# Performance work log

Measured on AMD Instinct MI355X. Metric: run time of the kernel, lower is better.

Reference implementation:

```python
import jax, jax.numpy as jnp
import numpy as np

N = 4096      # nodes
IN = 45       # input_dim
H = 44        # hidden_dim
NH = 4        # num_heads
HD = H // NH  # head_dim = 11
E = 131072    # edges
SCALE = 0.1
NEG = -1e9


def _linear_params(key, fan_in, fan_out):
    kw, kb = jax.random.split(key)
    s = 1.0 / np.sqrt(fan_in)
    W = jax.random.uniform(kw, (fan_in, fan_out), jnp.float32, -s, s)
    b = jax.random.uniform(kb, (fan_out,), jnp.float32, -s, s)
    return W, b


def setup_inputs() -> dict:
    key = jax.random.key(0)
    ks = jax.random.split(key, 9)
    node_features = jax.random.normal(ks[0], (N, IN), jnp.float32)
    edge_index = jax.random.randint(ks[1], (2, E), 0, N, jnp.int32)
    # dt_minutes must be nonnegative (sqrt); channel 1 unused by forward
    temporal_data = jax.random.uniform(ks[2], (N, N, 2), jnp.float32, 0.01, 60.0)
    Wp, bp = _linear_params(ks[3], IN, H)
    Wq, bq = _linear_params(ks[4], H, H)
    Wk, bk = _linear_params(ks[5], H, H)
    Wv, bv = _linear_params(ks[6], H, H)
    Wo, bo = _linear_params(ks[7], H, H)
    return dict(node_features=node_features, edge_index=edge_index,
                temporal_data=temporal_data, Wp=Wp, bp=bp, Wq=Wq, bq=bq,
                Wk=Wk, bk=bk, Wv=Wv, bv=bv, Wo=Wo, bo=bo)


def reference(node_features, edge_index, temporal_data,
              Wp, bp, Wq, bq, Wk, bk, Wv, bv, Wo, bo):
    # input projection (N > 1000 so dag_positional_encoding is skipped)
    x = node_features @ Wp + bp                       # [N, H]
    # per-head QKV: [NH, N, HD]
    Q = (x @ Wq + bq).reshape(N, NH, HD).transpose(1, 0, 2)
    K = (x @ Wk + bk).reshape(N, NH, HD).transpose(1, 0, 2)
    V = (x @ Wv + bv).reshape(N, NH, HD).transpose(1, 0, 2)
    # edge mask: True blocks attention; edges and self-loops are allowed
    mask = jnp.ones((N, N), dtype=bool)
    mask = mask.at[edge_index[0], edge_index[1]].set(False)
    diag = jnp.arange(N)
    mask = mask.at[diag, diag].set(False)
    # rbf temporal bias: -sqrt(dt / (scale + 1e-6))
    tb = -jnp.sqrt(temporal_data[:, :, 0] / (SCALE + 1e-6))  # [N, N]
    scores = jnp.einsum('hnd,hmd->hnm', Q, K) / np.sqrt(HD)  # [NH, N, N]
    scores = scores + tb[None]
    scores = jnp.where(mask[None], NEG, scores)
    attn = jax.nn.softmax(scores, axis=-1)
    out = jnp.einsum('hnm,hmd->hnd', attn, V)                # [NH, N, HD]
    attended = out.transpose(1, 0, 2).reshape(N, H)          # [N, H]
    return attended @ Wo + bo
```

## Files before the change

kernel.cpp:

```cpp
#include <hip/hip_runtime.h>
#include <math.h>

#define NN 4096
#define INDIM 45
#define HH 44
#define NHEAD 4
#define HD 11
#define NEDGE 131072
#define CAP 128
#define MASKW (NN / 64)
#define NPB 8
#define RPITCH 66

typedef unsigned short ushort_t;

__device__ __forceinline__ float wsum64(float v) {
    #pragma unroll
    for (int i = 32; i > 0; i >>= 1) v += __shfl_xor(v, i, 64);
    return v;
}
__device__ __forceinline__ float wmax64(float v) {
    #pragma unroll
    for (int i = 32; i > 0; i >>= 1) v = fmaxf(v, __shfl_xor(v, i, 64));
    return v;
}
__device__ __forceinline__ ushort_t f2bf(float x) {
    unsigned u = __float_as_uint(x);
    u += 0x7FFFu + ((u >> 16) & 1u);
    return (ushort_t)(u >> 16);
}
__device__ __forceinline__ float bfl(unsigned u) { return __uint_as_float(u << 16); }
__device__ __forceinline__ float bfh(unsigned u) { return __uint_as_float(u & 0xFFFF0000u); }

__global__ __launch_bounds__(256)
void proj_zero(const float* __restrict__ nf,
               const float* __restrict__ Wp, const float* __restrict__ bp,
               const float* __restrict__ Wq, const float* __restrict__ bq,
               const float* __restrict__ Wk, const float* __restrict__ bk,
               const float* __restrict__ Wv, const float* __restrict__ bv,
               unsigned long long* __restrict__ mask,
               float* __restrict__ Qp, ushort_t* __restrict__ KVb) {
    const int tid = threadIdx.x;
    const int gsz = gridDim.x * 256;
    for (int i = blockIdx.x * 256 + tid; i < NN * MASKW; i += gsz) mask[i] = 0ull;

    __shared__ float xs[NPB][HH];
    const int n0 = blockIdx.x * NPB;
    for (int idx = tid; idx < NPB * HH; idx += 256) {
        int nl = idx / HH, j = idx - nl * HH;
        const float* row = nf + (size_t)(n0 + nl) * INDIM;
        float a = bp[j];
        #pragma unroll
        for (int k = 0; k < INDIM; ++k) a += row[k] * Wp[k * HH + j];
        xs[nl][j] = a;
    }
    __syncthreads();
    for (int idx = tid; idx < NPB * HH; idx += 256) {
        int nl = idx / HH, j = idx - nl * HH;
        const float* row = xs[nl];
        float aq = bq[j], ak = bk[j], av = bv[j];
        #pragma unroll
        for (int k = 0; k < HH; ++k) {
            float xv = row[k];
            aq += xv * Wq[k * HH + j];
            ak += xv * Wk[k * HH + j];
            av += xv * Wv[k * HH + j];
        }
        int h = j / HD, d = j - h * HD;
        size_t nh = (size_t)(n0 + nl) * NHEAD + h;
        Qp[nh * 12 + d]       = aq;
        KVb[nh * 24 + d]      = f2bf(ak);
        KVb[nh * 24 + 12 + d] = f2bf(av);
    }
}

__global__ __launch_bounds__(256)
void build_mask(const int* __restrict__ ei, unsigned long long* __restrict__ mask) {
    int i = blockIdx.x * blockDim.x + threadIdx.x;
    if (i < NEDGE) {
        int r = ei[i];
        int c = ei[NEDGE + i];
        atomicOr(&mask[(size_t)r * MASKW + (c >> 6)], 1ull << (c & 63));
    }
}

__global__ __launch_bounds__(256, 4)
void attn_out(const float* __restrict__ Qp, const ushort_t* __restrict__ KVb,
              const float* __restrict__ temporal,
              const unsigned long long* __restrict__ mask,
              const float* __restrict__ Wo, const float* __restrict__ bo,
              float* __restrict__ out) {
    const int tid = threadIdx.x;
    const int lane = tid & 63;
    const int h = tid >> 6;
    const int n = blockIdx.x;
    const float scale = 0.30151134457776363f;
    const float tbmul = 9.99990000099999f;

    __shared__ int cols_s[NHEAD][CAP];
    __shared__ float red_s[NHEAD][12][RPITCH];
    __shared__ float att_s[HH];

    unsigned long long w = mask[(size_t)n * MASKW + lane];
    if (lane == (n >> 6)) w |= 1ull << (n & 63);
    int c = __popcll(w);
    int inc = c;
    #pragma unroll
    for (int i = 1; i < 64; i <<= 1) {
        int v = __shfl_up(inc, i, 64);
        if (lane >= i) inc += v;
    }
    int off = inc - c;
    int deg = __shfl(inc, 63, 64);
    if (deg > CAP) deg = CAP;
    while (w) {
        int b = __builtin_ctzll(w);
        w &= w - 1;
        if (off < CAP) cols_s[h][off] = lane * 64 + b;
        ++off;
    }

    const float4* qp4 = (const float4*)(Qp + ((size_t)n * NHEAD + h) * 12);
    float4 q0 = qp4[0], q1 = qp4[1], q2 = qp4[2];

    if (deg <= 64) {
        const bool act = lane < deg;
        const int col = act ? cols_s[h][lane] : cols_s[h][0];
        float t = temporal[((size_t)n * NN + col) * 2];
        const uint4* kv4 = (const uint4*)(KVb + (size_t)(col * NHEAD + h) * 24);
        uint4 A = kv4[0], B = kv4[1], C = kv4[2];
        float s = q0.x*bfl(A.x) + q0.y*bfh(A.x) + q0.z*bfl(A.y) + q0.w*bfh(A.y)
                + q1.x*bfl(A.z) + q1.y*bfh(A.z) + q1.z*bfl(A.w) + q1.w*bfh(A.w)
                + q2.x*bfl(B.x) + q2.y*bfh(B.x) + q2.z*bfl(B.y);
        float p = act ? __expf(s * scale - sqrtf(t * tbmul)) : 0.f;
        float vv[11] = { bfl(B.z), bfh(B.z), bfl(B.w), bfh(B.w),
                         bfl(C.x), bfh(C.x), bfl(C.y), bfh(C.y),
                         bfl(C.z), bfh(C.z), bfl(C.w) };

        float* myred = &red_s[h][0][0];
        #pragma unroll
        for (int d = 0; d < HD; ++d) myred[d * RPITCH + lane] = p * vv[d];
        myred[11 * RPITCH + lane] = p;
        int dd = lane < 12 ? lane : 0;
        const float2* rp = (const float2*)(myred + dd * RPITCH);
        float sum = 0.f;
        #pragma unroll
        for (int i = 0; i < 32; ++i) { float2 v2 = rp[i]; sum += v2.x + v2.y; }
        float inv = 1.f / __shfl(sum, 11, 64);
        if (lane < HD) att_s[h * HD + lane] = sum * inv;
    } else {
        float mcur = -INFINITY, lsum = 0.f, oacc[HD];
        #pragma unroll
        for (int d = 0; d < HD; ++d) oacc[d] = 0.f;
        for (int base = 0; base < deg; base += 64) {
            const int jj = base + lane;
            const bool act = jj < deg;
            const int col = act ? cols_s[h][jj] : 0;
            float t = temporal[((size_t)n * NN + col) * 2];
            const uint4* kv4 = (const uint4*)(KVb + (size_t)(col * NHEAD + h) * 24);
            uint4 A = kv4[0], B = kv4[1], C = kv4[2];
            float s = q0.x*bfl(A.x) + q0.y*bfh(A.x) + q0.z*bfl(A.y) + q0.w*bfh(A.y)
                    + q1.x*bfl(A.z) + q1.y*bfh(A.z) + q1.z*bfl(A.w) + q1.w*bfh(A.w)
                    + q2.x*bfl(B.x) + q2.y*bfh(B.x) + q2.z*bfl(B.y);
            float vv[11] = { bfl(B.z), bfh(B.z), bfl(B.w), bfh(B.w),
                             bfl(C.x), bfh(C.x), bfl(C.y), bfh(C.y),
                             bfl(C.z), bfh(C.z), bfl(C.w) };
            if (act) {
                s = s * scale - sqrtf(t * tbmul);
                if (s > mcur) {
                    float f = __expf(mcur - s);
                    lsum *= f;
                    #pragma unroll
                    for (int d = 0; d < HD; ++d) oacc[d] *= f;
                    mcur = s;
                }
                float p = __expf(s - mcur);
                lsum += p;
                #pragma unroll
                for (int d = 0; d < HD; ++d) oacc[d] += p * vv[d];
            }
        }
        float M = wmax64(mcur);
        float sc = (mcur == -INFINITY) ? 0.f : __expf(mcur - M);
        float L = wsum64(lsum * sc);
        float inv = 1.f / L;
        #pragma unroll
        for (int d = 0; d < HD; ++d) {
            float o = wsum64(oacc[d] * sc);
            if (lane == d) att_s[h * HD + d] = o * inv;
        }
    }
    __syncthreads();

    if (tid < HH) {
        float a = bo[tid];
        #pragma unroll
        for (int k = 0; k < HH; ++k) a += att_s[k] * Wo[k * HH + tid];
        out[(size_t)n * HH + tid] = a;
    }
}

extern "C" void kernel_launch(void* const* d_in, const int* in_sizes, int n_in,
                              void* d_out, int out_size, void* d_ws, size_t ws_size,
                              hipStream_t stream) {
    const float* nf       = (const float*)d_in[0];
    const int*   ei       = (const int*)d_in[1];
    const float* temporal = (const float*)d_in[2];
    const float* Wp = (const float*)d_in[3];
    const float* bp = (const float*)d_in[4];
    const float* Wq = (const float*)d_in[5];
    const float* bq = (const float*)d_in[6];
    const float* Wk = (const float*)d_in[7];
    const float* bk = (const float*)d_in[8];
    const float* Wv = (const float*)d_in[9];
    const float* bv = (const float*)d_in[10];
    const float* Wo = (const float*)d_in[11];
    const float* bo = (const float*)d_in[12];
    float* outp = (float*)d_out;

    char* ws = (char*)d_ws;
    unsigned long long* mask = (unsigned long long*)ws;
    float*    Qp  = (float*)(ws + (2u << 20));
    ushort_t* KVb = (ushort_t*)(Qp + (size_t)NN * NHEAD * 12);

    proj_zero<<<NN / NPB, 256, 0, stream>>>(nf, Wp, bp, Wq, bq, Wk, bk, Wv, bv,
                                            mask, Qp, KVb);
    build_mask<<<(NEDGE + 255) / 256, 256, 0, stream>>>(ei, mask);
    attn_out<<<NN, 256, 0, stream>>>(Qp, KVb, temporal, mask, Wo, bo, outp);
}
```

Before: 33.63 us.

## Fold input projection into QKV weights and pad KV rows to 64 bytes

A new prep kernel multiplies Wp and the bias bp into the Q/K/V weight matrices, giving fused 46x44 weights. The projection kernel then runs one thread per (node, output), making a single 45-term pass instead of two dependent matmuls with a shared-memory staging step and a block barrier. The K/V bf16 row stride grows from 24 to 32 elements so each gathered row is 64-byte aligned, and the Q load is hoisted above the mask scan in the attention kernel. This adds a fourth kernel launch, and folding the weights changes the floating-point rounding slightly.

Result: slower. 37.49 us (+11.5%).

```diff
diff --git a/kernel.cpp b/kernel.cpp
--- a/kernel.cpp
+++ b/kernel.cpp
@@ -9,8 +9,8 @@
 #define NEDGE 131072
 #define CAP 128
 #define MASKW (NN / 64)
-#define NPB 8
 #define RPITCH 66
+#define KVSTRIDE 32
 
 typedef unsigned short ushort_t;
 
@@ -33,45 +33,58 @@
 __device__ __forceinline__ float bfh(unsigned u) { return __uint_as_float(u & 0xFFFF0000u); }
 
 __global__ __launch_bounds__(256)
-void proj_zero(const float* __restrict__ nf,
-               const float* __restrict__ Wp, const float* __restrict__ bp,
-               const float* __restrict__ Wq, const float* __restrict__ bq,
-               const float* __restrict__ Wk, const float* __restrict__ bk,
-               const float* __restrict__ Wv, const float* __restrict__ bv,
+void prep_w(const float* __restrict__ Wp, const float* __restrict__ bp,
+            const float* __restrict__ Wq, const float* __restrict__ bq,
+            const float* __restrict__ Wk, const float* __restrict__ bk,
+            const float* __restrict__ Wv, const float* __restrict__ bv,
+            float* __restrict__ Wf) {
+    int idx = blockIdx.x * 256 + threadIdx.x;
+    if (idx >= 3 * 46 * HH) return;
+    int mat = idx / (46 * HH);
+    int rem = idx - mat * 46 * HH;
+    int r = rem / HH, j = rem - r * HH;
+    const float* W = (mat == 0) ? Wq : (mat == 1) ? Wk : Wv;
+    const float* b = (mat == 0) ? bq : (mat == 1) ? bk : bv;
+    float a;
+    if (r < INDIM) {
+        a = 0.f;
+        #pragma unroll
+        for (int m = 0; m < HH; ++m) a += Wp[r * HH + m] * W[m * HH + j];
+    } else {
+        a = b[j];
+        #pragma unroll
+        for (int m = 0; m < HH; ++m) a += bp[m] * W[m * HH + j];
+    }
+    Wf[idx] = a;
+}
+
+__global__ __launch_bounds__(256)
+void proj_zero(const float* __restrict__ nf, const float* __restrict__ Wf,
                unsigned long long* __restrict__ mask,
                float* __restrict__ Qp, ushort_t* __restrict__ KVb) {
-    const int tid = threadIdx.x;
+    const int tid = blockIdx.x * 256 + threadIdx.x;
     const int gsz = gridDim.x * 256;
-    for (int i = blockIdx.x * 256 + tid; i < NN * MASKW; i += gsz) mask[i] = 0ull;
-
-    __shared__ float xs[NPB][HH];
-    const int n0 = blockIdx.x * NPB;
-    for (int idx = tid; idx < NPB * HH; idx += 256) {
-        int nl = idx / HH, j = idx - nl * HH;
-        const float* row = nf + (size_t)(n0 + nl) * INDIM;
-        float a = bp[j];
-        #pragma unroll
-        for (int k = 0; k < INDIM; ++k) a += row[k] * Wp[k * HH + j];
-        xs[nl][j] = a;
-    }
-    __syncthreads();
-    for (int idx = tid; idx < NPB * HH; idx += 256) {
-        int nl = idx / HH, j = idx - nl * HH;
-        const float* row = xs[nl];
-        float aq = bq[j], ak = bk[j], av = bv[j];
-        #pragma unroll
-        for (int k = 0; k < HH; ++k) {
-            float xv = row[k];
-            aq += xv * Wq[k * HH + j];
-            ak += xv * Wk[k * HH + j];
-            av += xv * Wv[k * HH + j];
-        }
-        int h = j / HD, d = j - h * HD;
-        size_t nh = (size_t)(n0 + nl) * NHEAD + h;
-        Qp[nh * 12 + d]       = aq;
-        KVb[nh * 24 + d]      = f2bf(ak);
-        KVb[nh * 24 + 12 + d] = f2bf(av);
-    }
+    for (int i = tid; i < NN * MASKW; i += gsz) mask[i] = 0ull;
+
+    if (tid >= NN * HH) return;
+    int n = tid / HH, j = tid - n * HH;
+    const float* row = nf + (size_t)n * INDIM;
+    const float* Wfq = Wf;
+    const float* Wfk = Wf + 46 * HH;
+    const float* Wfv = Wf + 2 * 46 * HH;
+    float aq = Wfq[INDIM * HH + j], ak = Wfk[INDIM * HH + j], av = Wfv[INDIM * HH + j];
+    #pragma unroll
+    for (int k = 0; k < INDIM; ++k) {
+        float xv = row[k];
+        aq += xv * Wfq[k * HH + j];
+        ak += xv * Wfk[k * HH + j];
+        av += xv * Wfv[k * HH + j];
+    }
+    int h = j / HD, d = j - h * HD;
+    size_t nh = (size_t)n * NHEAD + h;
+    Qp[nh * 12 + d]             = aq;
+    KVb[nh * KVSTRIDE + d]      = f2bf(ak);
+    KVb[nh * KVSTRIDE + 12 + d] = f2bf(av);
 }
 
 __global__ __launch_bounds__(256)
@@ -101,6 +114,9 @@
     __shared__ float red_s[NHEAD][12][RPITCH];
     __shared__ float att_s[HH];
 
+    const float4* qp4 = (const float4*)(Qp + ((size_t)n * NHEAD + h) * 12);
+    float4 q0 = qp4[0], q1 = qp4[1], q2 = qp4[2];
+
     unsigned long long w = mask[(size_t)n * MASKW + lane];
     if (lane == (n >> 6)) w |= 1ull << (n & 63);
     int c = __popcll(w);
@@ -120,14 +136,11 @@
         ++off;
     }
 
-    const float4* qp4 = (const float4*)(Qp + ((size_t)n * NHEAD + h) * 12);
-    float4 q0 = qp4[0], q1 = qp4[1], q2 = qp4[2];
-
     if (deg <= 64) {
         const bool act = lane < deg;
         const int col = act ? cols_s[h][lane] : cols_s[h][0];
         float t = temporal[((size_t)n * NN + col) * 2];
-        const uint4* kv4 = (const uint4*)(KVb + (size_t)(col * NHEAD + h) * 24);
+        const uint4* kv4 = (const uint4*)(KVb + (size_t)(col * NHEAD + h) * KVSTRIDE);
         uint4 A = kv4[0], B = kv4[1], C = kv4[2];
         float s = q0.x*bfl(A.x) + q0.y*bfh(A.x) + q0.z*bfl(A.y) + q0.w*bfh(A.y)
                 + q1.x*bfl(A.z) + q1.y*bfh(A.z) + q1.z*bfl(A.w) + q1.w*bfh(A.w)
@@ -157,7 +170,7 @@
             const bool act = jj < deg;
             const int col = act ? cols_s[h][jj] : 0;
             float t = temporal[((size_t)n * NN + col) * 2];
-            const uint4* kv4 = (const uint4*)(KVb + (size_t)(col * NHEAD + h) * 24);
+            const uint4* kv4 = (const uint4*)(KVb + (size_t)(col * NHEAD + h) * KVSTRIDE);
             uint4 A = kv4[0], B = kv4[1], C = kv4[2];
             float s = q0.x*bfl(A.x) + q0.y*bfh(A.x) + q0.z*bfl(A.y) + q0.w*bfh(A.y)
                     + q1.x*bfl(A.z) + q1.y*bfh(A.z) + q1.z*bfl(A.w) + q1.w*bfh(A.w)
@@ -220,11 +233,12 @@
 
     char* ws = (char*)d_ws;
     unsigned long long* mask = (unsigned long long*)ws;
-    float*    Qp  = (float*)(ws + (2u << 20));
+    float*    Wf  = (float*)(ws + (2u << 20));
+    float*    Qp  = Wf + 3 * 46 * HH;
     ushort_t* KVb = (ushort_t*)(Qp + (size_t)NN * NHEAD * 12);
 
-    proj_zero<<<NN / NPB, 256, 0, stream>>>(nf, Wp, bp, Wq, bq, Wk, bk, Wv, bv,
-                                            mask, Qp, KVb);
+    prep_w<<<(3 * 46 * HH + 255) / 256, 256, 0, stream>>>(Wp, bp, Wq, bq, Wk, bk, Wv, bv, Wf);
+    proj_zero<<<(NN * HH + 255) / 256, 256, 0, stream>>>(nf, Wf, mask, Qp, KVb);
     build_mask<<<(NEDGE + 255) / 256, 256, 0, stream>>>(ei, mask);
     attn_out<<<NN, 256, 0, stream>>>(Qp, KVb, temporal, mask, Wo, bo, outp);
 }
```
